# Kernel tuning notes

Hardware: AMD Instinct MI355X
Metric: run time of the kernel (lower is better)

## Reference

```python
import jax, jax.numpy as jnp
import numpy as np

# Production-scale dims: total AST nodes, total CFG nodes, number of mapping pairs
N_AST, N_CFG, M = 500_000, 100_000, 400_000
D_AST, D_CFG = 256, 256


def setup_inputs() -> dict:
    key = jax.random.key(0)
    ks = jax.random.split(key, 6)
    prev = jax.random.normal(ks[0], (N_AST, D_AST), jnp.float32)
    cfg = jax.random.normal(ks[1], (N_CFG, D_CFG), jnp.float32)
    # unique key indices (a random subset of AST node ids) -> deterministic scatter
    key_indices = jax.random.permutation(ks[2], N_AST)[:M].astype(jnp.int32)
    value_indices = jax.random.randint(ks[3], (M,), 0, N_CFG, jnp.int32)
    s_u = 1.0 / np.sqrt(D_CFG)
    W_update = jax.random.uniform(ks[4], (D_CFG, D_AST), jnp.float32, -s_u, s_u)
    b_update = jnp.zeros((D_AST,), jnp.float32)
    s_g = 1.0 / np.sqrt(2 * D_AST)
    W_gate = jax.random.uniform(ks[5], (2 * D_AST, D_AST), jnp.float32, -s_g, s_g)
    b_gate = jnp.zeros((D_AST,), jnp.float32)
    return dict(
        previous_ast_nodes_encodings=prev,
        new_cfg_nodes_encodings=cfg,
        key_indices=key_indices,
        value_indices=value_indices,
        W_update=W_update,
        b_update=b_update,
        W_gate=W_gate,
        b_gate=b_gate,
    )


def reference(previous_ast_nodes_encodings, new_cfg_nodes_encodings,
              key_indices, value_indices, W_update, b_update, W_gate, b_gate):
    # gather: rows of AST-node state and CFG-node updates participating in the mapping
    state = previous_ast_nodes_encodings[key_indices]      # [M, D_AST]
    upd = new_cfg_nodes_encodings[value_indices]           # [M, D_CFG]
    # StateUpdater (gated update; dropout is identity in eval mode)
    proj = jax.nn.relu(upd @ W_update + b_update)          # project update to state dim
    gate = jax.nn.sigmoid(jnp.concatenate([state, proj], axis=-1) @ W_gate + b_gate)
    new_state = gate * state + (1.0 - gate) * proj         # [M, D_AST]
    # scatter updated rows back into the full AST-node encodings tensor
    return previous_ast_nodes_encodings.at[key_indices].set(new_state)
```

## Files before the change

kernel.cpp:

```cpp
#include <hip/hip_runtime.h>
#include <hip/hip_bf16.h>

typedef __attribute__((ext_vector_type(8))) short short8;
typedef __attribute__((ext_vector_type(4))) float f32x4;
typedef __attribute__((ext_vector_type(4))) unsigned short u16x4;

#define D 256

static __device__ __forceinline__ unsigned short f2bf(float f) {
    union { __hip_bfloat16 h; unsigned short u; } v;
    v.h = __float2bfloat16(f);
    return v.u;
}
static __device__ __forceinline__ float bf2f(unsigned short h) {
    union { unsigned u; float f; } v; v.u = ((unsigned)h) << 16;
    return v.f;
}

__global__ void pack_w_kernel(const float* __restrict__ W, unsigned short* __restrict__ dst,
                              int log2nkk, int total) {
    int p = blockIdx.x * blockDim.x + threadIdx.x;
    if (p >= total) return;
    int j     = p & 7;
    int lane  = (p >> 3) & 63;
    int kk    = (p >> 9) & ((1 << log2nkk) - 1);
    int ntile = p >> (9 + log2nkk);
    int k = kk * 32 + ((lane >> 4) * 8) + j;
    int n = ntile * 16 + (lane & 15);
    dst[p] = f2bf(W[k * D + n]);
}

__global__ void clear_flags_kernel(unsigned* __restrict__ f, int n) {
    int i = blockIdx.x * blockDim.x + threadIdx.x;
    if (i < n) f[i] = 0u;
}

__global__ void scatter_flags_kernel(const int* __restrict__ kidx,
                                     unsigned char* __restrict__ flags, int m) {
    int i = blockIdx.x * blockDim.x + threadIdx.x;
    if (i < m) flags[kidx[i]] = 1;
}

__global__ __launch_bounds__(256, 5) void projall_kernel(
    const float* __restrict__ cfg, const unsigned short* __restrict__ WuP,
    const float* __restrict__ bu, unsigned short* __restrict__ projall, int ncfg)
{
    __shared__ unsigned short Aub[64 * D];
    char* aubB = (char*)Aub;
    const int t = threadIdx.x, lane = t & 63, wid = t >> 6;
    const int lr = lane & 15, lk = lane >> 4;
    const int base = blockIdx.x * 64;

    #pragma unroll
    for (int i = 0; i < 16; ++i) {
        int row = wid * 16 + i;
        int r = base + row;
        f32x4 u = (f32x4){0.f, 0.f, 0.f, 0.f};
        if (r < ncfg) u = *(const f32x4*)(cfg + (size_t)r * D + lane * 4);
        int boff = (lane * 8) ^ ((row & 7) << 4);
        u16x4 hu;
        hu.x = f2bf(u.x); hu.y = f2bf(u.y); hu.z = f2bf(u.z); hu.w = f2bf(u.w);
        *(u16x4*)(aubB + row * 512 + boff) = hu;
    }
    __syncthreads();

    f32x4 acc[4][4];
    #pragma unroll
    for (int fm = 0; fm < 4; ++fm)
        #pragma unroll
        for (int fn = 0; fn < 4; ++fn)
            acc[fm][fn] = (f32x4){0.f, 0.f, 0.f, 0.f};

    #pragma unroll
    for (int kk = 0; kk < 8; ++kk) {
        short8 a[4], b[4];
        #pragma unroll
        for (int fm = 0; fm < 4; ++fm) {
            int row = fm * 16 + lr;
            int boff = (kk * 64 + lk * 16) ^ ((row & 7) << 4);
            a[fm] = *(const short8*)(aubB + row * 512 + boff);
        }
        #pragma unroll
        for (int fn = 0; fn < 4; ++fn) {
            int ntile = wid * 4 + fn;
            b[fn] = *(const short8*)(WuP + ((size_t)(ntile * 8 + kk) * 64 + lane) * 8);
        }
        #pragma unroll
        for (int fm = 0; fm < 4; ++fm)
            #pragma unroll
            for (int fn = 0; fn < 4; ++fn)
                acc[fm][fn] = __builtin_amdgcn_mfma_f32_16x16x32_bf16(a[fm], b[fn], acc[fm][fn], 0, 0, 0);
    }

    float bu4[4];
    #pragma unroll
    for (int fn = 0; fn < 4; ++fn) bu4[fn] = bu[wid * 64 + fn * 16 + lr];

    #pragma unroll
    for (int fm = 0; fm < 4; ++fm) {
        #pragma unroll
        for (int i = 0; i < 4; ++i) {
            int r = base + fm * 16 + lk * 4 + i;
            if (r >= ncfg) continue;
            #pragma unroll
            for (int fn = 0; fn < 4; ++fn) {
                float p = acc[fm][fn][i] + bu4[fn];
                p = p > 0.f ? p : 0.f;
                projall[(size_t)r * D + wid * 64 + fn * 16 + lr] = f2bf(p);
            }
        }
    }
}

__global__ __launch_bounds__(1024, 8) void fused4_kernel(
    const float* __restrict__ prev, const unsigned short* __restrict__ projall,
    const int* __restrict__ kidx, const int* __restrict__ vidx,
    const unsigned short* __restrict__ WgP, const float* __restrict__ bg,
    float* __restrict__ out, const unsigned char* __restrict__ flags,
    int nrows, int rpb)
{
    __shared__ unsigned short Ast[64 * D];
    __shared__ unsigned short Apj[64 * D];
    char* astB = (char*)Ast;
    char* apjB = (char*)Apj;

    const int tid  = threadIdx.x;
    const int lane = tid & 63;
    const int wid  = tid >> 6;
    const int lr   = lane & 15;
    const int lk   = lane >> 4;
    const int base = blockIdx.x * 64;

    #pragma unroll
    for (int i = 0; i < 4; ++i) {
        int row = wid * 4 + i;
        int kr = kidx[base + row];
        f32x4 s = __builtin_nontemporal_load((const f32x4*)(prev + (size_t)kr * D) + lane);
        int boff = (lane * 8) ^ ((row & 7) << 4);
        u16x4 hs;
        hs.x = f2bf(s.x); hs.y = f2bf(s.y); hs.z = f2bf(s.z); hs.w = f2bf(s.w);
        *(u16x4*)(astB + row * 512 + boff) = hs;
    }
    #pragma unroll
    for (int i = 0; i < 2; ++i) {
        int row = wid * 4 + i * 2 + (lane >> 5);
        int vr = vidx[base + row];
        short8 pv = *(const short8*)(projall + (size_t)vr * D + (lane & 31) * 8);
        int boff = ((lane & 31) * 16) ^ ((row & 7) << 4);
        *(short8*)(apjB + row * 512 + boff) = pv;
    }
    __syncthreads();

    f32x4 acc2[4];
    #pragma unroll
    for (int fm = 0; fm < 4; ++fm)
        acc2[fm] = (f32x4){0.f, 0.f, 0.f, 0.f};

    #pragma unroll
    for (int kk = 0; kk < 16; ++kk) {
        const char* Asrc = (kk < 8) ? astB : apjB;
        int kkl = kk & 7;
        short8 a[4], b;
        #pragma unroll
        for (int fm = 0; fm < 4; ++fm) {
            int row = fm * 16 + lr;
            int boff = (kkl * 64 + lk * 16) ^ ((row & 7) << 4);
            a[fm] = *(const short8*)(Asrc + row * 512 + boff);
        }
        b = *(const short8*)(WgP + ((size_t)(wid * 16 + kk) * 64 + lane) * 8);
        #pragma unroll
        for (int fm = 0; fm < 4; ++fm)
            acc2[fm] = __builtin_amdgcn_mfma_f32_16x16x32_bf16(a[fm], b, acc2[fm], 0, 0, 0);
    }

    const float bg1 = bg[wid * 16 + lr];
    const int col = wid * 16 + lr;

    #pragma unroll
    for (int fm = 0; fm < 4; ++fm) {
        #pragma unroll
        for (int i = 0; i < 4; ++i) {
            int row = fm * 16 + lk * 4 + i;
            int kr = kidx[base + row];
            float x = acc2[fm][i] + bg1;
            float g = 1.f / (1.f + __expf(-x));
            int boff = (col * 2) ^ ((row & 7) << 4);
            float st = bf2f(*(const unsigned short*)(astB + row * 512 + boff));
            float pj = bf2f(*(const unsigned short*)(apjB + row * 512 + boff));
            __builtin_nontemporal_store(g * st + (1.f - g) * pj, out + (size_t)kr * D + col);
        }
    }

    int start = blockIdx.x * rpb;
    int end = start + rpb; if (end > nrows) end = nrows;
    for (int row = start + wid; row < end; row += 16) {
        if (flags[row]) continue;
        size_t idx = (size_t)row * 64 + lane;
        f32x4 v = __builtin_nontemporal_load((const f32x4*)prev + idx);
        __builtin_nontemporal_store(v, (f32x4*)out + idx);
    }
}

extern "C" void kernel_launch(void* const* d_in, const int* in_sizes, int n_in,
                              void* d_out, int out_size, void* d_ws, size_t ws_size,
                              hipStream_t stream) {
    const float* prev = (const float*)d_in[0];
    const float* cfg  = (const float*)d_in[1];
    const int* kidx   = (const int*)d_in[2];
    const int* vidx   = (const int*)d_in[3];
    const float* Wu   = (const float*)d_in[4];
    const float* bu   = (const float*)d_in[5];
    const float* Wg   = (const float*)d_in[6];
    const float* bg   = (const float*)d_in[7];
    float* out = (float*)d_out;

    const int N_AST = in_sizes[0] / D;
    const int N_CFG = in_sizes[1] / D;
    const int M     = in_sizes[2];

    unsigned short* WuP = (unsigned short*)d_ws;
    unsigned short* WgP = WuP + 256 * 256;
    unsigned char* flags = (unsigned char*)(WgP + 512 * 256);
    unsigned short* projall = (unsigned short*)((char*)d_ws + (1 << 20));

    const int totalWu = 256 * 256;
    const int totalWg = 512 * 256;
    const int nflag4  = (N_AST + 3) / 4;
    const int ntiles  = M / 64;
    const int rpb     = (N_AST + ntiles - 1) / ntiles;

    pack_w_kernel<<<(totalWu + 255) / 256, 256, 0, stream>>>(Wu, WuP, 3, totalWu);
    pack_w_kernel<<<(totalWg + 255) / 256, 256, 0, stream>>>(Wg, WgP, 4, totalWg);
    clear_flags_kernel<<<(nflag4 + 255) / 256, 256, 0, stream>>>((unsigned*)flags, nflag4);
    scatter_flags_kernel<<<(M + 255) / 256, 256, 0, stream>>>(kidx, flags, M);

    projall_kernel<<<(N_CFG + 63) / 64, 256, 0, stream>>>(cfg, WuP, bu, projall, N_CFG);
    fused4_kernel<<<ntiles, 1024, 0, stream>>>(prev, projall, kidx, vidx, WgP, bg,
                                               out, flags, N_AST, rpb);
}
```

Before: 397.2 us.

## Process AST rows sequentially via inverse key-to-value map instead of scattered keys

Builds an inverse index mapping each AST row to its CFG value index (or -1), then launches the fused gate kernel over all AST rows in order. State loads and output stores become contiguous instead of random gathers/scatters, and the separate passthrough copy loop is folded into the epilogue. In exchange the gate GEMM is computed for unmapped rows too, adding compute, and passthrough values are read per-element from prev.

```diff
diff --git a/kernel.cpp b/kernel.cpp
--- a/kernel.cpp
+++ b/kernel.cpp
@@ -30,15 +30,15 @@
     dst[p] = f2bf(W[k * D + n]);
 }
 
-__global__ void clear_flags_kernel(unsigned* __restrict__ f, int n) {
+__global__ void clear_pvr_kernel(int* __restrict__ pvr, int n) {
     int i = blockIdx.x * blockDim.x + threadIdx.x;
-    if (i < n) f[i] = 0u;
-}
-
-__global__ void scatter_flags_kernel(const int* __restrict__ kidx,
-                                     unsigned char* __restrict__ flags, int m) {
+    if (i < n) pvr[i] = -1;
+}
+
+__global__ void scatter_pvr_kernel(const int* __restrict__ kidx, const int* __restrict__ vidx,
+                                   int* __restrict__ pvr, int m) {
     int i = blockIdx.x * blockDim.x + threadIdx.x;
-    if (i < m) flags[kidx[i]] = 1;
+    if (i < m) pvr[kidx[i]] = vidx[i];
 }
 
 __global__ __launch_bounds__(256, 5) void projall_kernel(
@@ -112,12 +112,10 @@
     }
 }
 
-__global__ __launch_bounds__(1024, 8) void fused4_kernel(
+__global__ __launch_bounds__(1024, 8) void fused5_kernel(
     const float* __restrict__ prev, const unsigned short* __restrict__ projall,
-    const int* __restrict__ kidx, const int* __restrict__ vidx,
-    const unsigned short* __restrict__ WgP, const float* __restrict__ bg,
-    float* __restrict__ out, const unsigned char* __restrict__ flags,
-    int nrows, int rpb)
+    const int* __restrict__ pvr, const unsigned short* __restrict__ WgP,
+    const float* __restrict__ bg, float* __restrict__ out, int nrows)
 {
     __shared__ unsigned short Ast[64 * D];
     __shared__ unsigned short Apj[64 * D];
@@ -134,8 +132,9 @@
     #pragma unroll
     for (int i = 0; i < 4; ++i) {
         int row = wid * 4 + i;
-        int kr = kidx[base + row];
-        f32x4 s = __builtin_nontemporal_load((const f32x4*)(prev + (size_t)kr * D) + lane);
+        int r = base + row;
+        f32x4 s = (f32x4){0.f, 0.f, 0.f, 0.f};
+        if (r < nrows) s = __builtin_nontemporal_load((const f32x4*)(prev + (size_t)r * D) + lane);
         int boff = (lane * 8) ^ ((row & 7) << 4);
         u16x4 hs;
         hs.x = f2bf(s.x); hs.y = f2bf(s.y); hs.z = f2bf(s.z); hs.w = f2bf(s.w);
@@ -144,10 +143,12 @@
     #pragma unroll
     for (int i = 0; i < 2; ++i) {
         int row = wid * 4 + i * 2 + (lane >> 5);
-        int vr = vidx[base + row];
-        short8 pv = *(const short8*)(projall + (size_t)vr * D + (lane & 31) * 8);
+        int r = base + row;
+        int pv = (r < nrows) ? pvr[r] : -1;
+        int src = pv < 0 ? 0 : pv;
+        short8 pvv = *(const short8*)(projall + (size_t)src * D + (lane & 31) * 8);
         int boff = ((lane & 31) * 16) ^ ((row & 7) << 4);
-        *(short8*)(apjB + row * 512 + boff) = pv;
+        *(short8*)(apjB + row * 512 + boff) = pvv;
     }
     __syncthreads();
 
@@ -181,23 +182,22 @@
         #pragma unroll
         for (int i = 0; i < 4; ++i) {
             int row = fm * 16 + lk * 4 + i;
-            int kr = kidx[base + row];
-            float x = acc2[fm][i] + bg1;
-            float g = 1.f / (1.f + __expf(-x));
-            int boff = (col * 2) ^ ((row & 7) << 4);
-            float st = bf2f(*(const unsigned short*)(astB + row * 512 + boff));
-            float pj = bf2f(*(const unsigned short*)(apjB + row * 512 + boff));
-            __builtin_nontemporal_store(g * st + (1.f - g) * pj, out + (size_t)kr * D + col);
-        }
-    }
-
-    int start = blockIdx.x * rpb;
-    int end = start + rpb; if (end > nrows) end = nrows;
-    for (int row = start + wid; row < end; row += 16) {
-        if (flags[row]) continue;
-        size_t idx = (size_t)row * 64 + lane;
-        f32x4 v = __builtin_nontemporal_load((const f32x4*)prev + idx);
-        __builtin_nontemporal_store(v, (f32x4*)out + idx);
+            int r = base + row;
+            if (r >= nrows) continue;
+            int pv = pvr[r];
+            float val;
+            if (pv >= 0) {
+                float x = acc2[fm][i] + bg1;
+                float g = 1.f / (1.f + __expf(-x));
+                int boff = (col * 2) ^ ((row & 7) << 4);
+                float st = bf2f(*(const unsigned short*)(astB + row * 512 + boff));
+                float pj = bf2f(*(const unsigned short*)(apjB + row * 512 + boff));
+                val = g * st + (1.f - g) * pj;
+            } else {
+                val = prev[(size_t)r * D + col];
+            }
+            __builtin_nontemporal_store(val, out + (size_t)r * D + col);
+        }
     }
 }
 
@@ -220,21 +220,18 @@
 
     unsigned short* WuP = (unsigned short*)d_ws;
     unsigned short* WgP = WuP + 256 * 256;
-    unsigned char* flags = (unsigned char*)(WgP + 512 * 256);
-    unsigned short* projall = (unsigned short*)((char*)d_ws + (1 << 20));
+    int* pvr = (int*)((char*)d_ws + (384 << 10));
+    unsigned short* projall = (unsigned short*)((char*)d_ws + (4 << 20));
 
     const int totalWu = 256 * 256;
     const int totalWg = 512 * 256;
-    const int nflag4  = (N_AST + 3) / 4;
-    const int ntiles  = M / 64;
-    const int rpb     = (N_AST + ntiles - 1) / ntiles;
+    const int ntiles  = (N_AST + 63) / 64;
 
     pack_w_kernel<<<(totalWu + 255) / 256, 256, 0, stream>>>(Wu, WuP, 3, totalWu);
     pack_w_kernel<<<(totalWg + 255) / 256, 256, 0, stream>>>(Wg, WgP, 4, totalWg);
-    clear_flags_kernel<<<(nflag4 + 255) / 256, 256, 0, stream>>>((unsigned*)flags, nflag4);
-    scatter_flags_kernel<<<(M + 255) / 256, 256, 0, stream>>>(kidx, flags, M);
+    clear_pvr_kernel<<<(N_AST + 255) / 256, 256, 0, stream>>>(pvr, N_AST);
+    scatter_pvr_kernel<<<(M + 255) / 256, 256, 0, stream>>>(kidx, vidx, pvr, M);
 
     projall_kernel<<<(N_CFG + 63) / 64, 256, 0, stream>>>(cfg, WuP, bu, projall, N_CFG);
-    fused4_kernel<<<ntiles, 1024, 0, stream>>>(prev, projall, kidx, vidx, WgP, bg,
-                                               out, flags, N_AST, rpb);
-}
+    fused5_kernel<<<ntiles, 1024, 0, stream>>>(prev, projall, pvr, WgP, bg, out, N_AST);
+}
```

Result: slower. 559.3 us (+40.8%).

## Make fused gate kernel persistent with register prefetch of next tile

Applied to the files above, without the earlier changes.

The fused gate/blend kernel now launches a fixed grid of 512 blocks that loop over the 64-row tiles instead of one block per tile. While the current tile's MFMA and epilogue run, the next tile's gathered prev rows and projected rows are loaded into registers, which is meant to hide gather latency. The copy-through range per block is resized to match the smaller grid. The costs are fewer resident blocks (1024-thread blocks with 64 KB of LDS each), extra live registers, and a second barrier per tile. The projall workspace offset is also moved.

```diff
diff --git a/kernel.cpp b/kernel.cpp
--- a/kernel.cpp
+++ b/kernel.cpp
@@ -112,12 +112,12 @@
     }
 }
 
-__global__ __launch_bounds__(1024, 8) void fused4_kernel(
+__global__ __launch_bounds__(1024, 8) void fused6_kernel(
     const float* __restrict__ prev, const unsigned short* __restrict__ projall,
     const int* __restrict__ kidx, const int* __restrict__ vidx,
     const unsigned short* __restrict__ WgP, const float* __restrict__ bg,
     float* __restrict__ out, const unsigned char* __restrict__ flags,
-    int nrows, int rpb)
+    int ntiles, int nrows, int rpb)
 {
     __shared__ unsigned short Ast[64 * D];
     __shared__ unsigned short Apj[64 * D];
@@ -129,66 +129,101 @@
     const int wid  = tid >> 6;
     const int lr   = lane & 15;
     const int lk   = lane >> 4;
-    const int base = blockIdx.x * 64;
-
-    #pragma unroll
-    for (int i = 0; i < 4; ++i) {
-        int row = wid * 4 + i;
-        int kr = kidx[base + row];
-        f32x4 s = __builtin_nontemporal_load((const f32x4*)(prev + (size_t)kr * D) + lane);
-        int boff = (lane * 8) ^ ((row & 7) << 4);
-        u16x4 hs;
-        hs.x = f2bf(s.x); hs.y = f2bf(s.y); hs.z = f2bf(s.z); hs.w = f2bf(s.w);
-        *(u16x4*)(astB + row * 512 + boff) = hs;
-    }
-    #pragma unroll
-    for (int i = 0; i < 2; ++i) {
-        int row = wid * 4 + i * 2 + (lane >> 5);
-        int vr = vidx[base + row];
-        short8 pv = *(const short8*)(projall + (size_t)vr * D + (lane & 31) * 8);
-        int boff = ((lane & 31) * 16) ^ ((row & 7) << 4);
-        *(short8*)(apjB + row * 512 + boff) = pv;
-    }
-    __syncthreads();
-
-    f32x4 acc2[4];
-    #pragma unroll
-    for (int fm = 0; fm < 4; ++fm)
-        acc2[fm] = (f32x4){0.f, 0.f, 0.f, 0.f};
-
-    #pragma unroll
-    for (int kk = 0; kk < 16; ++kk) {
-        const char* Asrc = (kk < 8) ? astB : apjB;
-        int kkl = kk & 7;
-        short8 a[4], b;
-        #pragma unroll
-        for (int fm = 0; fm < 4; ++fm) {
-            int row = fm * 16 + lr;
-            int boff = (kkl * 64 + lk * 16) ^ ((row & 7) << 4);
-            a[fm] = *(const short8*)(Asrc + row * 512 + boff);
-        }
-        b = *(const short8*)(WgP + ((size_t)(wid * 16 + kk) * 64 + lane) * 8);
-        #pragma unroll
-        for (int fm = 0; fm < 4; ++fm)
-            acc2[fm] = __builtin_amdgcn_mfma_f32_16x16x32_bf16(a[fm], b, acc2[fm], 0, 0, 0);
-    }
-
+    const int step = gridDim.x;
     const float bg1 = bg[wid * 16 + lr];
     const int col = wid * 16 + lr;
 
-    #pragma unroll
-    for (int fm = 0; fm < 4; ++fm) {
+    f32x4  sreg[4];
+    short8 preg[2];
+
+    {
+        const int base = blockIdx.x * 64;
         #pragma unroll
         for (int i = 0; i < 4; ++i) {
-            int row = fm * 16 + lk * 4 + i;
-            int kr = kidx[base + row];
-            float x = acc2[fm][i] + bg1;
-            float g = 1.f / (1.f + __expf(-x));
-            int boff = (col * 2) ^ ((row & 7) << 4);
-            float st = bf2f(*(const unsigned short*)(astB + row * 512 + boff));
-            float pj = bf2f(*(const unsigned short*)(apjB + row * 512 + boff));
-            __builtin_nontemporal_store(g * st + (1.f - g) * pj, out + (size_t)kr * D + col);
-        }
+            int kr = kidx[base + wid * 4 + i];
+            sreg[i] = __builtin_nontemporal_load((const f32x4*)(prev + (size_t)kr * D) + lane);
+        }
+        #pragma unroll
+        for (int i = 0; i < 2; ++i) {
+            int row = wid * 4 + i * 2 + (lane >> 5);
+            int vr = vidx[base + row];
+            preg[i] = *(const short8*)(projall + (size_t)vr * D + (lane & 31) * 8);
+        }
+    }
+
+    for (int t = blockIdx.x; t < ntiles; t += step) {
+        const int base = t * 64;
+
+        #pragma unroll
+        for (int i = 0; i < 4; ++i) {
+            int row = wid * 4 + i;
+            int boff = (lane * 8) ^ ((row & 7) << 4);
+            u16x4 hs;
+            hs.x = f2bf(sreg[i].x); hs.y = f2bf(sreg[i].y);
+            hs.z = f2bf(sreg[i].z); hs.w = f2bf(sreg[i].w);
+            *(u16x4*)(astB + row * 512 + boff) = hs;
+        }
+        #pragma unroll
+        for (int i = 0; i < 2; ++i) {
+            int row = wid * 4 + i * 2 + (lane >> 5);
+            int boff = ((lane & 31) * 16) ^ ((row & 7) << 4);
+            *(short8*)(apjB + row * 512 + boff) = preg[i];
+        }
+        __syncthreads();
+
+        int tn = t + step;
+        if (tn < ntiles) {
+            int nbase = tn * 64;
+            #pragma unroll
+            for (int i = 0; i < 4; ++i) {
+                int kr = kidx[nbase + wid * 4 + i];
+                sreg[i] = __builtin_nontemporal_load((const f32x4*)(prev + (size_t)kr * D) + lane);
+            }
+            #pragma unroll
+            for (int i = 0; i < 2; ++i) {
+                int row = wid * 4 + i * 2 + (lane >> 5);
+                int vr = vidx[nbase + row];
+                preg[i] = *(const short8*)(projall + (size_t)vr * D + (lane & 31) * 8);
+            }
+        }
+
+        f32x4 acc2[4];
+        #pragma unroll
+        for (int fm = 0; fm < 4; ++fm)
+            acc2[fm] = (f32x4){0.f, 0.f, 0.f, 0.f};
+
+        #pragma unroll
+        for (int kk = 0; kk < 16; ++kk) {
+            const char* Asrc = (kk < 8) ? astB : apjB;
+            int kkl = kk & 7;
+            short8 a[4], b;
+            #pragma unroll
+            for (int fm = 0; fm < 4; ++fm) {
+                int row = fm * 16 + lr;
+                int boff = (kkl * 64 + lk * 16) ^ ((row & 7) << 4);
+                a[fm] = *(const short8*)(Asrc + row * 512 + boff);
+            }
+            b = *(const short8*)(WgP + ((size_t)(wid * 16 + kk) * 64 + lane) * 8);
+            #pragma unroll
+            for (int fm = 0; fm < 4; ++fm)
+                acc2[fm] = __builtin_amdgcn_mfma_f32_16x16x32_bf16(a[fm], b, acc2[fm], 0, 0, 0);
+        }
+
+        #pragma unroll
+        for (int fm = 0; fm < 4; ++fm) {
+            #pragma unroll
+            for (int i = 0; i < 4; ++i) {
+                int row = fm * 16 + lk * 4 + i;
+                int kr = kidx[base + row];
+                float x = acc2[fm][i] + bg1;
+                float g = 1.f / (1.f + __expf(-x));
+                int boff = (col * 2) ^ ((row & 7) << 4);
+                float st = bf2f(*(const unsigned short*)(astB + row * 512 + boff));
+                float pj = bf2f(*(const unsigned short*)(apjB + row * 512 + boff));
+                __builtin_nontemporal_store(g * st + (1.f - g) * pj, out + (size_t)kr * D + col);
+            }
+        }
+        __syncthreads();
     }
 
     int start = blockIdx.x * rpb;
@@ -221,13 +256,14 @@
     unsigned short* WuP = (unsigned short*)d_ws;
     unsigned short* WgP = WuP + 256 * 256;
     unsigned char* flags = (unsigned char*)(WgP + 512 * 256);
-    unsigned short* projall = (unsigned short*)((char*)d_ws + (1 << 20));
+    unsigned short* projall = (unsigned short*)((char*)d_ws + (4 << 20));
 
     const int totalWu = 256 * 256;
     const int totalWg = 512 * 256;
     const int nflag4  = (N_AST + 3) / 4;
     const int ntiles  = M / 64;
-    const int rpb     = (N_AST + ntiles - 1) / ntiles;
+    const int nblocks = 512;
+    const int rpb     = (N_AST + nblocks - 1) / nblocks;
 
     pack_w_kernel<<<(totalWu + 255) / 256, 256, 0, stream>>>(Wu, WuP, 3, totalWu);
     pack_w_kernel<<<(totalWg + 255) / 256, 256, 0, stream>>>(Wg, WgP, 4, totalWg);
@@ -235,6 +271,6 @@
     scatter_flags_kernel<<<(M + 255) / 256, 256, 0, stream>>>(kidx, flags, M);
 
     projall_kernel<<<(N_CFG + 63) / 64, 256, 0, stream>>>(cfg, WuP, bu, projall, N_CFG);
-    fused4_kernel<<<ntiles, 1024, 0, stream>>>(prev, projall, kidx, vidx, WgP, bg,
-                                               out, flags, N_AST, rpb);
-}
+    fused6_kernel<<<nblocks, 1024, 0, stream>>>(prev, projall, kidx, vidx, WgP, bg,
+                                                out, flags, ntiles, N_AST, rpb);
+}
```

Result: slower. 1.118 ms (+181.6%).

## Stage fp32 state rows via direct global-to-LDS loads and exact-precision blend

Applied to the files above, without the earlier changes.

The fused gate kernel now loads the gathered fp32 state rows straight into LDS with global_load_lds (XOR-swizzled), converting to bf16 only when it builds the MFMA operands. The final blend therefore uses the exact fp32 state. The tile shrinks to 32 rows and 512 threads, with each wave computing a 2x2 MFMA fragment instead of 1x4, and the projall workspace offset moves. The aim is to skip the register round-trip for the state gather and raise occupancy with smaller blocks, at the cost of more LDS per row and repeated bf16 conversion inside the k-loop.

```diff
diff --git a/kernel.cpp b/kernel.cpp
--- a/kernel.cpp
+++ b/kernel.cpp
@@ -112,16 +112,15 @@
     }
 }
 
-__global__ __launch_bounds__(1024, 8) void fused4_kernel(
+__global__ __launch_bounds__(512, 6) void fused7_kernel(
     const float* __restrict__ prev, const unsigned short* __restrict__ projall,
     const int* __restrict__ kidx, const int* __restrict__ vidx,
     const unsigned short* __restrict__ WgP, const float* __restrict__ bg,
     float* __restrict__ out, const unsigned char* __restrict__ flags,
     int nrows, int rpb)
 {
-    __shared__ unsigned short Ast[64 * D];
-    __shared__ unsigned short Apj[64 * D];
-    char* astB = (char*)Ast;
+    __shared__ float          Sst[32 * D];
+    __shared__ unsigned short Apj[32 * D];
     char* apjB = (char*)Apj;
 
     const int tid  = threadIdx.x;
@@ -129,17 +128,17 @@
     const int wid  = tid >> 6;
     const int lr   = lane & 15;
     const int lk   = lane >> 4;
-    const int base = blockIdx.x * 64;
+    const int base = blockIdx.x * 32;
 
     #pragma unroll
     for (int i = 0; i < 4; ++i) {
         int row = wid * 4 + i;
         int kr = kidx[base + row];
-        f32x4 s = __builtin_nontemporal_load((const f32x4*)(prev + (size_t)kr * D) + lane);
-        int boff = (lane * 8) ^ ((row & 7) << 4);
-        u16x4 hs;
-        hs.x = f2bf(s.x); hs.y = f2bf(s.y); hs.z = f2bf(s.z); hs.w = f2bf(s.w);
-        *(u16x4*)(astB + row * 512 + boff) = hs;
+        const float* gsrc = prev + (size_t)kr * D + ((lane ^ (row & 7)) << 2);
+        __builtin_amdgcn_global_load_lds(
+            (const __attribute__((address_space(1))) unsigned*)gsrc,
+            (__attribute__((address_space(3))) unsigned*)&Sst[row * D],
+            16, 0, 0);
     }
     #pragma unroll
     for (int i = 0; i < 2; ++i) {
@@ -151,49 +150,89 @@
     }
     __syncthreads();
 
-    f32x4 acc2[4];
-    #pragma unroll
-    for (int fm = 0; fm < 4; ++fm)
-        acc2[fm] = (f32x4){0.f, 0.f, 0.f, 0.f};
-
-    #pragma unroll
-    for (int kk = 0; kk < 16; ++kk) {
-        const char* Asrc = (kk < 8) ? astB : apjB;
-        int kkl = kk & 7;
-        short8 a[4], b;
-        #pragma unroll
-        for (int fm = 0; fm < 4; ++fm) {
+    f32x4 acc2[2][2];
+    #pragma unroll
+    for (int fm = 0; fm < 2; ++fm)
+        #pragma unroll
+        for (int fn = 0; fn < 2; ++fn)
+            acc2[fm][fn] = (f32x4){0.f, 0.f, 0.f, 0.f};
+
+    #pragma unroll
+    for (int kk = 0; kk < 8; ++kk) {
+        short8 a[2], b[2];
+        #pragma unroll
+        for (int fm = 0; fm < 2; ++fm) {
             int row = fm * 16 + lr;
-            int boff = (kkl * 64 + lk * 16) ^ ((row & 7) << 4);
-            a[fm] = *(const short8*)(Asrc + row * 512 + boff);
-        }
-        b = *(const short8*)(WgP + ((size_t)(wid * 16 + kk) * 64 + lane) * 8);
-        #pragma unroll
-        for (int fm = 0; fm < 4; ++fm)
-            acc2[fm] = __builtin_amdgcn_mfma_f32_16x16x32_bf16(a[fm], b, acc2[fm], 0, 0, 0);
-    }
-
-    const float bg1 = bg[wid * 16 + lr];
-    const int col = wid * 16 + lr;
-
-    #pragma unroll
-    for (int fm = 0; fm < 4; ++fm) {
+            int c0 = (kk * 8 + lk * 2) ^ (row & 7);
+            int c1 = (kk * 8 + lk * 2 + 1) ^ (row & 7);
+            f32x4 v0 = *(const f32x4*)&Sst[row * D + c0 * 4];
+            f32x4 v1 = *(const f32x4*)&Sst[row * D + c1 * 4];
+            short8 af;
+            af[0] = (short)f2bf(v0.x); af[1] = (short)f2bf(v0.y);
+            af[2] = (short)f2bf(v0.z); af[3] = (short)f2bf(v0.w);
+            af[4] = (short)f2bf(v1.x); af[5] = (short)f2bf(v1.y);
+            af[6] = (short)f2bf(v1.z); af[7] = (short)f2bf(v1.w);
+            a[fm] = af;
+        }
+        #pragma unroll
+        for (int fn = 0; fn < 2; ++fn) {
+            int ntile = wid * 2 + fn;
+            b[fn] = *(const short8*)(WgP + ((size_t)(ntile * 16 + kk) * 64 + lane) * 8);
+        }
+        #pragma unroll
+        for (int fm = 0; fm < 2; ++fm)
+            #pragma unroll
+            for (int fn = 0; fn < 2; ++fn)
+                acc2[fm][fn] = __builtin_amdgcn_mfma_f32_16x16x32_bf16(a[fm], b[fn], acc2[fm][fn], 0, 0, 0);
+    }
+    #pragma unroll
+    for (int kk = 0; kk < 8; ++kk) {
+        short8 a[2], b[2];
+        #pragma unroll
+        for (int fm = 0; fm < 2; ++fm) {
+            int row = fm * 16 + lr;
+            int boff = (kk * 64 + lk * 16) ^ ((row & 7) << 4);
+            a[fm] = *(const short8*)(apjB + row * 512 + boff);
+        }
+        #pragma unroll
+        for (int fn = 0; fn < 2; ++fn) {
+            int ntile = wid * 2 + fn;
+            b[fn] = *(const short8*)(WgP + ((size_t)(ntile * 16 + kk + 8) * 64 + lane) * 8);
+        }
+        #pragma unroll
+        for (int fm = 0; fm < 2; ++fm)
+            #pragma unroll
+            for (int fn = 0; fn < 2; ++fn)
+                acc2[fm][fn] = __builtin_amdgcn_mfma_f32_16x16x32_bf16(a[fm], b[fn], acc2[fm][fn], 0, 0, 0);
+    }
+
+    float bg2[2];
+    #pragma unroll
+    for (int fn = 0; fn < 2; ++fn) bg2[fn] = bg[wid * 32 + fn * 16 + lr];
+
+    #pragma unroll
+    for (int fm = 0; fm < 2; ++fm) {
         #pragma unroll
         for (int i = 0; i < 4; ++i) {
             int row = fm * 16 + lk * 4 + i;
             int kr = kidx[base + row];
-            float x = acc2[fm][i] + bg1;
-            float g = 1.f / (1.f + __expf(-x));
-            int boff = (col * 2) ^ ((row & 7) << 4);
-            float st = bf2f(*(const unsigned short*)(astB + row * 512 + boff));
-            float pj = bf2f(*(const unsigned short*)(apjB + row * 512 + boff));
-            __builtin_nontemporal_store(g * st + (1.f - g) * pj, out + (size_t)kr * D + col);
+            float* orow = out + (size_t)kr * D;
+            #pragma unroll
+            for (int fn = 0; fn < 2; ++fn) {
+                int col = wid * 32 + fn * 16 + lr;
+                float x = acc2[fm][fn][i] + bg2[fn];
+                float g = 1.f / (1.f + __expf(-x));
+                float st = Sst[row * D + (((col >> 2) ^ (row & 7)) << 2) + (col & 3)];
+                int pboff = (col * 2) ^ ((row & 7) << 4);
+                float pj = bf2f(*(const unsigned short*)(apjB + row * 512 + pboff));
+                __builtin_nontemporal_store(g * st + (1.f - g) * pj, orow + col);
+            }
         }
     }
 
     int start = blockIdx.x * rpb;
     int end = start + rpb; if (end > nrows) end = nrows;
-    for (int row = start + wid; row < end; row += 16) {
+    for (int row = start + wid; row < end; row += 8) {
         if (flags[row]) continue;
         size_t idx = (size_t)row * 64 + lane;
         f32x4 v = __builtin_nontemporal_load((const f32x4*)prev + idx);
@@ -221,12 +260,12 @@
     unsigned short* WuP = (unsigned short*)d_ws;
     unsigned short* WgP = WuP + 256 * 256;
     unsigned char* flags = (unsigned char*)(WgP + 512 * 256);
-    unsigned short* projall = (unsigned short*)((char*)d_ws + (1 << 20));
+    unsigned short* projall = (unsigned short*)((char*)d_ws + (4 << 20));
 
     const int totalWu = 256 * 256;
     const int totalWg = 512 * 256;
     const int nflag4  = (N_AST + 3) / 4;
-    const int ntiles  = M / 64;
+    const int ntiles  = M / 32;
     const int rpb     = (N_AST + ntiles - 1) / ntiles;
 
     pack_w_kernel<<<(totalWu + 255) / 256, 256, 0, stream>>>(Wu, WuP, 3, totalWu);
@@ -235,6 +274,6 @@
     scatter_flags_kernel<<<(M + 255) / 256, 256, 0, stream>>>(kidx, flags, M);
 
     projall_kernel<<<(N_CFG + 63) / 64, 256, 0, stream>>>(cfg, WuP, bu, projall, N_CFG);
-    fused4_kernel<<<ntiles, 1024, 0, stream>>>(prev, projall, kidx, vidx, WgP, bg,
-                                               out, flags, N_AST, rpb);
-}
+    fused7_kernel<<<ntiles, 512, 0, stream>>>(prev, projall, kidx, vidx, WgP, bg,
+                                              out, flags, N_AST, rpb);
+}
```

After: 462.2 us. 1.16x slower.
